# Optimization experiments

Hardware: AMD Instinct MI355X
Metric: run time of the kernel (lower is better)

## Reference

```python
import jax, jax.numpy as jnp
import numpy as np

HOP = jnp.array([0, 1, 4, 7, 2, 5, 8, 3, 6, 9, 11, 14, 10, 12, 15, 13, 16])
GRAPH = jnp.array([0, 1, 4, 7, 2, 5, 8, 3, 6, 9, 12, 10, 13, 15, 11, 14, 16])
D_MODEL, L, D_INNER, D_STATE, DT_RANK = 512, 17, 1024, 4, 32


def layernorm(x, w, b, eps=1e-5):
    mu = x.mean(-1, keepdims=True)
    var = ((x - mu) ** 2).mean(-1, keepdims=True)
    return (x - mu) * jax.lax.rsqrt(var + eps) * w + b


def setup_inputs() -> dict:
    key = jax.random.key(0)
    ks = jax.random.split(key, 9)
    B = 4096
    s = lambda k, shape: jax.random.normal(k, shape, jnp.float32) * 0.02
    # A_log init per mamba_ssm: log(1..d_state) repeated over d_inner
    A_log = jnp.log(jnp.broadcast_to(jnp.arange(1, D_STATE + 1, dtype=jnp.float32), (D_INNER, D_STATE)))
    return {
        "x": jax.random.normal(ks[0], (B, L, D_MODEL), jnp.float32),
        "bp_embed": s(ks[1], (1, 5, D_MODEL)),
        "ln_w": jnp.ones((D_MODEL,), jnp.float32),
        "ln_b": jnp.zeros((D_MODEL,), jnp.float32),
        "in_proj_w": s(ks[2], (2 * D_INNER, D_MODEL)),
        "conv_w": 1.0 + s(ks[3], (D_INNER,)),  # d_conv=1 depthwise conv == per-channel scale
        "conv_b": jnp.zeros((D_INNER,), jnp.float32),
        "x_proj_w": s(ks[4], (DT_RANK + 2 * D_STATE, D_INNER)),
        "dt_proj_w": s(ks[5], (D_INNER, DT_RANK)),
        "dt_proj_b": s(ks[6], (D_INNER,)) - 4.0,  # softplus-inverse-ish small dt init
        "A_log": A_log,
        "D": jnp.ones((D_INNER,), jnp.float32),
        "out_proj_w": s(ks[7], (D_MODEL, D_INNER)),
    }


def mamba(u, in_proj_w, conv_w, conv_b, x_proj_w, dt_proj_w, dt_proj_b, A_log, D, out_proj_w):
    # u: [B, L, d_model]
    xz = jnp.einsum('bld,ed->ble', u, in_proj_w)          # [B,L,2*d_inner]
    xm, z = jnp.split(xz, 2, axis=-1)
    xm = jax.nn.silu(xm * conv_w + conv_b)                 # d_conv=1 -> pointwise
    x_dbl = jnp.einsum('ble,fe->blf', xm, x_proj_w)        # [B,L,dt_rank+2*d_state]
    dt_r = x_dbl[..., :DT_RANK]
    Bm = x_dbl[..., DT_RANK:DT_RANK + D_STATE]
    Cm = x_dbl[..., DT_RANK + D_STATE:]
    dt = jax.nn.softplus(jnp.einsum('blr,er->ble', dt_r, dt_proj_w) + dt_proj_b)  # [B,L,d_inner]
    A = -jnp.exp(A_log)                                    # [d_inner,d_state]

    def step(h, inp):
        dt_t, B_t, C_t, x_t = inp                          # [B,di],[B,ds],[B,ds],[B,di]
        dA = jnp.exp(dt_t[..., None] * A)                  # [B,di,ds]
        h = dA * h + (dt_t * x_t)[..., None] * B_t[:, None, :]
        y = jnp.einsum('bes,bs->be', h, C_t)
        return h, y

    bsz = u.shape[0]
    h0 = jnp.zeros((bsz, D_INNER, D_STATE), u.dtype)
    seq = (dt.transpose(1, 0, 2), Bm.transpose(1, 0, 2), Cm.transpose(1, 0, 2), xm.transpose(1, 0, 2))
    _, ys = jax.lax.scan(step, h0, seq)                    # ys: [L,B,d_inner]
    y = ys.transpose(1, 0, 2) + xm * D
    y = y * jax.nn.silu(z)
    return jnp.einsum('ble,de->bld', y, out_proj_w)


def reference(x, bp_embed, ln_w, ln_b, in_proj_w, conv_w, conv_b, x_proj_w,
              dt_proj_w, dt_proj_b, A_log, D, out_proj_w):
    bp = bp_embed
    x_bpe = jnp.concatenate([bp[:, :3], bp[:, :3], bp[:, :3], bp[:, :1],
                             bp[:, 3:], bp[:, :1], bp[:, 3:], bp[:, 3:]], axis=1)  # [1,17,dim]
    x_ssm = x[:, HOP, :] + x_bpe
    x_ssm = layernorm(x_ssm, ln_w, ln_b)
    x_ssm = mamba(x_ssm, in_proj_w, conv_w, conv_b, x_proj_w,
                  dt_proj_w, dt_proj_b, A_log, D, out_proj_w)
    return x + x_ssm[:, GRAPH, :]
```

## Files before the change

kernel.cpp:

```cpp
#include <hip/hip_runtime.h>

typedef unsigned short u16;
typedef unsigned int   u32;
typedef __bf16 bf16_t;
typedef bf16_t bf16x8 __attribute__((ext_vector_type(8)));
typedef float  f32x4  __attribute__((ext_vector_type(4)));

#define DEV static __device__ __forceinline__

__constant__ int c_HOP[17] = {0,1,4,7,2,5,8,3,6,9,11,14,10,12,15,13,16};
__constant__ int c_BPE[17] = {0,1,2,0,1,2,0,1,2,0,3,4,0,3,4,3,4};

DEV u16 f2bf(float f){
  u32 x = __builtin_bit_cast(u32, f);
  x += 0x7fffu + ((x >> 16) & 1u);
  return (u16)(x >> 16);
}
DEV float bf2f(u32 u){ return __builtin_bit_cast(float, u << 16); }
DEV float silu_f(float v){ return v / (1.f + __expf(-v)); }
DEV float softplus_f(float s){ return (s > 20.f) ? s : log1pf(__expf(s)); }

DEV void gll16(const void* g, void* l){
  __builtin_amdgcn_global_load_lds((__attribute__((address_space(1))) void*)g,
                                   (__attribute__((address_space(3))) void*)l,
                                   16, 0, 0);
}

__global__ __launch_bounds__(256) void cvt4(
    const float* __restrict__ s0, u16* __restrict__ d0, int n0,
    const float* __restrict__ s1, u16* __restrict__ d1, int n1,
    const float* __restrict__ s2, u16* __restrict__ d2, int n2,
    const float* __restrict__ s3, u16* __restrict__ d3, int n3)
{
  int t = blockIdx.x * 256 + threadIdx.x;
  if (t < n0){ d0[t] = f2bf(s0[t]); return; }
  t -= n0; if (t < n1){ d1[t] = f2bf(s1[t]); return; }
  t -= n1; if (t < n2){ d2[t] = f2bf(s2[t]); return; }
  t -= n2; if (t < n3){ d3[t] = f2bf(s3[t]); }
}

__global__ __launch_bounds__(256) void ln_gather(
    const float* __restrict__ x, const float* __restrict__ bpe,
    const float* __restrict__ lnw, const float* __restrict__ lnb,
    u16* __restrict__ u)
{
  int tok = blockIdx.x;
  int b = tok / 17;
  int l = tok - b * 17;
  const float* xr = x   + ((size_t)b * 17 + c_HOP[l]) * 512;
  const float* br = bpe + (size_t)c_BPE[l] * 512;
  int tid = threadIdx.x;
  int d0 = tid * 2;
  float2 xv = *(const float2*)(xr + d0);
  float2 bv = *(const float2*)(br + d0);
  float v0 = xv.x + bv.x, v1 = xv.y + bv.y;

  __shared__ float red[8];
  float s = v0 + v1;
  #pragma unroll
  for (int o = 32; o; o >>= 1) s += __shfl_xor(s, o);
  if ((tid & 63) == 0) red[tid >> 6] = s;
  __syncthreads();
  float mu = (red[0] + red[1] + red[2] + red[3]) * (1.f / 512.f);
  float a0 = v0 - mu, a1 = v1 - mu;
  float q = a0 * a0 + a1 * a1;
  #pragma unroll
  for (int o = 32; o; o >>= 1) q += __shfl_xor(q, o);
  if ((tid & 63) == 0) red[4 + (tid >> 6)] = q;
  __syncthreads();
  float var = (red[4] + red[5] + red[6] + red[7]) * (1.f / 512.f);
  float rs = rsqrtf(var + 1e-5f);

  u16 o0 = f2bf(a0 * rs * lnw[d0]     + lnb[d0]);
  u16 o1 = f2bf(a1 * rs * lnw[d0 + 1] + lnb[d0 + 1]);
  u32 pack = (u32)o0 | ((u32)o1 << 16);
  *(u32*)(u + (size_t)tok * 512 + d0) = pack;
}

enum { EPI_SPLIT = 0, EPI_OUT = 1 };

template<int EPI>
__global__ __launch_bounds__(512, 2) void gemm256(
    const u16* __restrict__ A, int lda,
    const u16* __restrict__ W, int K, int MT,
    u16* __restrict__ ob0, u16* __restrict__ ob1,
    const float* __restrict__ p0, const float* __restrict__ p1,
    const float* __restrict__ xres, float* __restrict__ fout)
{
  __shared__ u16 smem[65536];

  int nwg = gridDim.x;
  int cpx = nwg >> 3;
  int wg = (blockIdx.x & 7) * cpx + (blockIdx.x >> 3);
  int NT = nwg / MT;
  int nt = wg % NT, mt = wg / NT;
  int brow = mt * 256, bcol = nt * 256;
  int tid = threadIdx.x, lane = tid & 63, wid = tid >> 6;
  int wm = wid >> 2, wn = wid & 3;
  int l15 = lane & 15, lhi = lane >> 4;

  f32x4 acc[8][4] = {};

  int sr0 = tid >> 2, sr1 = 128 + (tid >> 2), sch = tid & 3;
  const u16* gA0 = A + (size_t)(brow + sr0) * lda + (sch ^ ((sr0 >> 1) & 3)) * 8;
  const u16* gA1 = A + (size_t)(brow + sr1) * lda + (sch ^ ((sr1 >> 1) & 3)) * 8;
  const u16* gW0 = W + (size_t)(bcol + sr0) * K   + (sch ^ ((sr0 >> 1) & 3)) * 8;
  const u16* gW1 = W + (size_t)(bcol + sr1) * K   + (sch ^ ((sr1 >> 1) & 3)) * 8;

  auto stA = [&](int buf, int kh, int koff) {
    char* d = (char*)smem + (buf * 2 + kh) * 16384 + tid * 16;
    gll16(gA0 + koff, d);
    gll16(gA1 + koff, d + 8192);
  };
  auto stB = [&](int buf, int kh, int koff) {
    char* d = (char*)smem + 65536 + (buf * 2 + kh) * 16384 + tid * 16;
    gll16(gW0 + koff, d);
    gll16(gW1 + koff, d + 8192);
  };

  int aoff[2][4], boff[4];
  #pragma unroll
  for (int mh = 0; mh < 2; mh++)
    #pragma unroll
    for (int mi = 0; mi < 4; mi++) {
      int r = wm * 128 + mh * 64 + mi * 16 + l15;
      aoff[mh][mi] = r * 64 + ((lhi ^ ((r >> 1) & 3)) * 16);
    }
  #pragma unroll
  for (int ni = 0; ni < 4; ni++) {
    int r = wn * 64 + ni * 16 + l15;
    boff[ni] = r * 64 + ((lhi ^ ((r >> 1) & 3)) * 16);
  }

  bf16x8 bvv[4];

#define PH(BUF, KH, MH, LOADB, STMT, WAIT)                                  \
  {                                                                         \
    const char* la = (const char*)smem + ((BUF) * 2 + (KH)) * 16384;        \
    bf16x8 a0 = *(const bf16x8*)(la + aoff[MH][0]);                         \
    bf16x8 a1 = *(const bf16x8*)(la + aoff[MH][1]);                         \
    bf16x8 a2 = *(const bf16x8*)(la + aoff[MH][2]);                         \
    bf16x8 a3 = *(const bf16x8*)(la + aoff[MH][3]);                         \
    if (LOADB) {                                                            \
      const char* lb = (const char*)smem + 65536 + ((BUF) * 2 + (KH)) * 16384; \
      bvv[0] = *(const bf16x8*)(lb + boff[0]);                              \
      bvv[1] = *(const bf16x8*)(lb + boff[1]);                              \
      bvv[2] = *(const bf16x8*)(lb + boff[2]);                              \
      bvv[3] = *(const bf16x8*)(lb + boff[3]);                              \
    }                                                                       \
    STMT                                                                    \
    __builtin_amdgcn_sched_barrier(0);                                      \
    __builtin_amdgcn_s_barrier();                                           \
    __builtin_amdgcn_s_setprio(1);                                          \
    acc[(MH)*4+0][0] = __builtin_amdgcn_mfma_f32_16x16x32_bf16(a0, bvv[0], acc[(MH)*4+0][0],0,0,0); \
    acc[(MH)*4+1][0] = __builtin_amdgcn_mfma_f32_16x16x32_bf16(a1, bvv[0], acc[(MH)*4+1][0],0,0,0); \
    acc[(MH)*4+2][0] = __builtin_amdgcn_mfma_f32_16x16x32_bf16(a2, bvv[0], acc[(MH)*4+2][0],0,0,0); \
    acc[(MH)*4+3][0] = __builtin_amdgcn_mfma_f32_16x16x32_bf16(a3, bvv[0], acc[(MH)*4+3][0],0,0,0); \
    acc[(MH)*4+0][1] = __builtin_amdgcn_mfma_f32_16x16x32_bf16(a0, bvv[1], acc[(MH)*4+0][1],0,0,0); \
    acc[(MH)*4+1][1] = __builtin_amdgcn_mfma_f32_16x16x32_bf16(a1, bvv[1], acc[(MH)*4+1][1],0,0,0); \
    acc[(MH)*4+2][1] = __builtin_amdgcn_mfma_f32_16x16x32_bf16(a2, bvv[1], acc[(MH)*4+2][1],0,0,0); \
    acc[(MH)*4+3][1] = __builtin_amdgcn_mfma_f32_16x16x32_bf16(a3, bvv[1], acc[(MH)*4+3][1],0,0,0); \
    acc[(MH)*4+0][2] = __builtin_amdgcn_mfma_f32_16x16x32_bf16(a0, bvv[2], acc[(MH)*4+0][2],0,0,0); \
    acc[(MH)*4+1][2] = __builtin_amdgcn_mfma_f32_16x16x32_bf16(a1, bvv[2], acc[(MH)*4+1][2],0,0,0); \
    acc[(MH)*4+2][2] = __builtin_amdgcn_mfma_f32_16x16x32_bf16(a2, bvv[2], acc[(MH)*4+2][2],0,0,0); \
    acc[(MH)*4+3][2] = __builtin_amdgcn_mfma_f32_16x16x32_bf16(a3, bvv[2], acc[(MH)*4+3][2],0,0,0); \
    acc[(MH)*4+0][3] = __builtin_amdgcn_mfma_f32_16x16x32_bf16(a0, bvv[3], acc[(MH)*4+0][3],0,0,0); \
    acc[(MH)*4+1][3] = __builtin_amdgcn_mfma_f32_16x16x32_bf16(a1, bvv[3], acc[(MH)*4+1][3],0,0,0); \
    acc[(MH)*4+2][3] = __builtin_amdgcn_mfma_f32_16x16x32_bf16(a2, bvv[3], acc[(MH)*4+2][3],0,0,0); \
    acc[(MH)*4+3][3] = __builtin_amdgcn_mfma_f32_16x16x32_bf16(a3, bvv[3], acc[(MH)*4+3][3],0,0,0); \
    __builtin_amdgcn_s_setprio(0);                                          \
    WAIT                                                                    \
    __builtin_amdgcn_s_barrier();                                           \
    __builtin_amdgcn_sched_barrier(0);                                      \
  }

  int T = K >> 6;

  stA(0, 0, 0);  stB(0, 0, 0);
  stA(0, 1, 32); stB(0, 1, 32);
  asm volatile("s_waitcnt vmcnt(4)" ::: "memory");
  __builtin_amdgcn_s_barrier();
  __builtin_amdgcn_sched_barrier(0);

  for (int t = 0; t < T; ++t) {
    int bf = t & 1, nb = bf ^ 1;
    int nk = (t + 1) << 6;
    bool s = (t + 1 < T);
    PH(bf, 0, 0, true,  { if (s) stA(nb, 0, nk); }, {});
    if (s) {
      PH(bf, 0, 1, false, { stB(nb, 0, nk); },
         { asm volatile("s_waitcnt vmcnt(4)" ::: "memory"); });
    } else {
      PH(bf, 0, 1, false, {},
         { asm volatile("s_waitcnt vmcnt(0)" ::: "memory"); });
    }
    PH(bf, 1, 0, true,  { if (s) stA(nb, 1, nk + 32); }, {});
    if (s) {
      PH(bf, 1, 1, false, { stB(nb, 1, nk + 32); },
         { asm volatile("s_waitcnt vmcnt(4)" ::: "memory"); });
    } else {
      PH(bf, 1, 1, false, {}, {});
    }
  }
#undef PH

  if constexpr (EPI == EPI_SPLIT) {
    u16* cl = smem;
    bool isx = (bcol < 1024);
    #pragma unroll
    for (int fm = 0; fm < 8; fm++) {
      int lrow = wm * 128 + fm * 16 + lhi * 4;
      #pragma unroll
      for (int ni = 0; ni < 4; ni++) {
        int col = wn * 64 + ni * 16 + l15;
        int cidx = isx ? (bcol + col) : 0;
        float cw = isx ? p0[cidx] : 1.f;
        float cb = isx ? p1[cidx] : 0.f;
        #pragma unroll
        for (int rr = 0; rr < 4; rr++) {
          int row = lrow + rr;
          cl[row * 256 + ((col + row * 8) & 255)] =
              f2bf(silu_f(acc[fm][ni][rr] * cw + cb));
        }
      }
    }
    __syncthreads();
    int colbase = isx ? bcol : (bcol - 1024);
    u16* dst = isx ? ob0 : ob1;
    #pragma unroll
    for (int i = 0; i < 16; i++) {
      int idx = i * 512 + tid;
      int row = idx >> 5;
      int q = idx & 31;
      uint4 v = *(const uint4*)(cl + row * 256 + ((q * 8 + row * 8) & 255));
      *(uint4*)(dst + (size_t)(brow + row) * 1024 + colbase + q * 8) = v;
    }
  } else {
    float* cf = (float*)smem;
    #pragma unroll
    for (int mh = 0; mh < 2; mh++) {
      __syncthreads();
      if (wm == mh) {
        #pragma unroll
        for (int fm = 0; fm < 8; fm++) {
          int lrow = fm * 16 + lhi * 4;
          #pragma unroll
          for (int ni = 0; ni < 4; ni++) {
            int col = wn * 64 + ni * 16 + l15;
            #pragma unroll
            for (int rr = 0; rr < 4; rr++) {
              int row = lrow + rr;
              cf[row * 256 + ((col + row * 4) & 255)] = acc[fm][ni][rr];
            }
          }
        }
      }
      __syncthreads();
      #pragma unroll
      for (int i = 0; i < 16; i++) {
        int idx = i * 512 + tid;
        int row = idx >> 6;
        int q = idx & 63;
        int grow = brow + mh * 128 + row;
        u32 bq = (u32)grow / 17u;
        int gl = grow - (int)bq * 17;
        size_t orow = (size_t)bq * 17 + c_HOP[gl];
        size_t off = orow * 512 + bcol + q * 4;
        float4 xv = *(const float4*)(xres + off);
        const float* cp = cf + row * 256 + ((q * 4 + row * 4) & 255);
        float4 ov;
        ov.x = xv.x + cp[0]; ov.y = xv.y + cp[1];
        ov.z = xv.z + cp[2]; ov.w = xv.w + cp[3];
        *(float4*)(fout + off) = ov;
      }
    }
  }
}

enum { EPI_XDBL = 0, EPI_DT = 1 };

template<int EPI>
__global__ __launch_bounds__(256) void gemm_bt(
    const u16* __restrict__ A, int lda,
    const u16* __restrict__ W, int K, int MT,
    u16* __restrict__ ob0, const float* __restrict__ p0)
{
  __shared__ u16 sm[16384];
  int nwg = gridDim.x;
  int cpx = nwg >> 3;
  int wg = (blockIdx.x & 7) * cpx + (blockIdx.x >> 3);
  int NT = nwg / MT;
  int nt = wg % NT, mt = wg / NT;
  int brow = mt * 128, bcol = nt * 128;
  int tid = threadIdx.x, lane = tid & 63, wid = tid >> 6;
  int wm = wid >> 1, wn = wid & 1;

  f32x4 acc[4][4] = {};

  int srow = tid >> 2;
  int sch  = tid & 3;

  const u16* gA0 = A + (size_t)(brow + srow)      * lda + (sch ^ ((srow >> 1) & 3)) * 8;
  const u16* gA1 = A + (size_t)(brow + 64 + srow) * lda + (sch ^ (((64 + srow) >> 1) & 3)) * 8;
  const u16* gW0 = W + (size_t)(bcol + srow)      * K   + (sch ^ ((srow >> 1) & 3)) * 8;
  const u16* gW1 = W + (size_t)(bcol + 64 + srow) * K   + (sch ^ (((64 + srow) >> 1) & 3)) * 8;

  auto STAGE = [&](int buf, int kt) {
    char* dA = (char*)sm + buf * 8192 + tid * 16;
    char* dW = (char*)sm + 16384 + buf * 8192 + tid * 16;
    gll16(gA0 + kt, dA);
    gll16(gA1 + kt, dA + 4096);
    gll16(gW0 + kt, dW);
    gll16(gW1 + kt, dW + 4096);
  };

  int aoff[4], boff[4];
  #pragma unroll
  for (int mi = 0; mi < 4; mi++) {
    int r = wm * 64 + mi * 16 + (lane & 15);
    aoff[mi] = r * 64 + (((lane >> 4) ^ ((r >> 1) & 3)) * 16);
  }
  #pragma unroll
  for (int ni = 0; ni < 4; ni++) {
    int r = wn * 64 + ni * 16 + (lane & 15);
    boff[ni] = r * 64 + (((lane >> 4) ^ ((r >> 1) & 3)) * 16);
  }

  auto COMPUTE = [&](int buf) {
    const char* la = (const char*)sm + buf * 8192;
    const char* lb = (const char*)sm + 16384 + buf * 8192;
    bf16x8 av[4], bv[4];
    #pragma unroll
    for (int mi = 0; mi < 4; mi++)
      av[mi] = *(const bf16x8*)(la + aoff[mi]);
    #pragma unroll
    for (int ni = 0; ni < 4; ni++)
      bv[ni] = *(const bf16x8*)(lb + boff[ni]);
    #pragma unroll
    for (int mi = 0; mi < 4; mi++)
      #pragma unroll
      for (int ni = 0; ni < 4; ni++)
        acc[mi][ni] = __builtin_amdgcn_mfma_f32_16x16x32_bf16(
            av[mi], bv[ni], acc[mi][ni], 0, 0, 0);
  };

  int nsteps = K >> 5;
  STAGE(0, 0);
  __syncthreads();
  int cur = 0;
  for (int s = 1; s < nsteps; ++s) {
    STAGE(cur ^ 1, s << 5);
    COMPUTE(cur);
    __syncthreads();
    cur ^= 1;
  }
  COMPUTE(cur);

  int r4 = (lane >> 4) * 4;
  int cl15 = lane & 15;
  if constexpr (EPI == EPI_XDBL) {
    #pragma unroll
    for (int mi = 0; mi < 4; mi++) {
      int rowb = brow + wm * 64 + mi * 16 + r4;
      #pragma unroll
      for (int ni = 0; ni < 4; ni++) {
        int col = bcol + wn * 64 + ni * 16 + cl15;
        if (col < 40) {
          #pragma unroll
          for (int rr = 0; rr < 4; rr++)
            ob0[(size_t)(rowb + rr) * 40 + col] = f2bf(acc[mi][ni][rr]);
        }
      }
    }
  } else {
    __syncthreads();
    u16* cls = sm;
    #pragma unroll
    for (int mi = 0; mi < 4; mi++) {
      int lrow = wm * 64 + mi * 16 + r4;
      #pragma unroll
      for (int ni = 0; ni < 4; ni++) {
        int lcol = wn * 64 + ni * 16 + cl15;
        float bb = p0[bcol + lcol];
        #pragma unroll
        for (int rr = 0; rr < 4; rr++) {
          int row = lrow + rr;
          cls[row * 128 + ((lcol + row * 8) & 127)] =
              f2bf(softplus_f(acc[mi][ni][rr] + bb));
        }
      }
    }
    __syncthreads();
    #pragma unroll
    for (int i = 0; i < 8; i++) {
      int idx = i * 256 + tid;
      int row = idx >> 4;
      int q = idx & 15;
      uint4 v = *(const uint4*)(cls + row * 128 + ((q * 8 + row * 8) & 127));
      *(uint4*)(ob0 + (size_t)(brow + row) * 1024 + bcol + q * 8) = v;
    }
  }
}

__global__ __launch_bounds__(128) void scan5(
    const u16* __restrict__ xm, const u16* __restrict__ zs,
    const u16* __restrict__ xdbl, u16* __restrict__ dty,
    const float* __restrict__ A_log, const float* __restrict__ Dp)
{
  int b = blockIdx.x;
  int tid = threadIdx.x;
  int e0 = tid * 8;
  const size_t base = (size_t)b * 17 * 1024;

  float4 al = *(const float4*)(A_log + (size_t)e0 * 4);
  float A0 = -__expf(al.x), A1 = -__expf(al.y);
  float A2 = -__expf(al.z), A3 = -__expf(al.w);
  float Dv[8];
  *(float4*)(Dv)     = *(const float4*)(Dp + e0);
  *(float4*)(Dv + 4) = *(const float4*)(Dp + e0 + 4);

  const u16* xmb = xm + base + e0;
  const u16* zsb = zs + base + e0;
  u16* db = dty + base + e0;
  const u16* bcb = xdbl + (size_t)b * 680 + 32;

  float h[8][4];
  #pragma unroll
  for (int c = 0; c < 8; c++)
    #pragma unroll
    for (int s = 0; s < 4; s++) h[c][s] = 0.f;

  #pragma unroll
  for (int t = 0; t < 17; t++) {
    uint4 xr = *(const uint4*)(xmb + t * 1024);
    uint4 zr = *(const uint4*)(zsb + t * 1024);
    uint4 dr = *(const uint4*)(db + t * 1024);
    uint4 bc = *(const uint4*)(bcb + t * 40);
    float B0 = bf2f(bc.x & 0xffffu), B1 = bf2f(bc.x >> 16);
    float B2 = bf2f(bc.y & 0xffffu), B3 = bf2f(bc.y >> 16);
    float C0 = bf2f(bc.z & 0xffffu), C1 = bf2f(bc.z >> 16);
    float C2 = bf2f(bc.w & 0xffffu), C3 = bf2f(bc.w >> 16);
    u32 yo[4];
    const u32* xw = (const u32*)&xr;
    const u32* zw = (const u32*)&zr;
    const u32* dw = (const u32*)&dr;
    #pragma unroll
    for (int c = 0; c < 8; c++) {
      u32 x16 = (c & 1) ? (xw[c >> 1] >> 16) : (xw[c >> 1] & 0xffffu);
      u32 z16 = (c & 1) ? (zw[c >> 1] >> 16) : (zw[c >> 1] & 0xffffu);
      u32 d16 = (c & 1) ? (dw[c >> 1] >> 16) : (dw[c >> 1] & 0xffffu);
      float xv = bf2f(x16), zv = bf2f(z16), dtv = bf2f(d16);
      float dx = dtv * xv;
      h[c][0] = __expf(dtv * A0) * h[c][0] + dx * B0;
      h[c][1] = __expf(dtv * A1) * h[c][1] + dx * B1;
      h[c][2] = __expf(dtv * A2) * h[c][2] + dx * B2;
      h[c][3] = __expf(dtv * A3) * h[c][3] + dx * B3;
      float yv = h[c][0] * C0 + h[c][1] * C1 + h[c][2] * C2 + h[c][3] * C3;
      u16 pk = f2bf((yv + xv * Dv[c]) * zv);
      if (c & 1) yo[c >> 1] |= ((u32)pk << 16);
      else       yo[c >> 1] = (u32)pk;
    }
    *(uint4*)(db + t * 1024) = *(uint4*)yo;
  }
}

extern "C" void kernel_launch(void* const* d_in, const int* in_sizes, int n_in,
                              void* d_out, int out_size, void* d_ws, size_t ws_size,
                              hipStream_t stream) {
  const float* x     = (const float*)d_in[0];
  const float* bpe   = (const float*)d_in[1];
  const float* lnw   = (const float*)d_in[2];
  const float* lnb   = (const float*)d_in[3];
  const float* w_in  = (const float*)d_in[4];
  const float* convw = (const float*)d_in[5];
  const float* convb = (const float*)d_in[6];
  const float* w_xp  = (const float*)d_in[7];
  const float* w_dt  = (const float*)d_in[8];
  const float* b_dt  = (const float*)d_in[9];
  const float* A_log = (const float*)d_in[10];
  const float* Dp    = (const float*)d_in[11];
  const float* w_out = (const float*)d_in[12];
  float* out = (float*)d_out;

  u16* ws = (u16*)d_ws;
  u16* wb_in  = ws;
  u16* wb_out = wb_in  + 1048576;
  u16* wb_xp  = wb_out + 524288;
  u16* wb_dt  = wb_xp  + 40960;
  u16* xm     = wb_dt  + 32768;
  u16* zs     = xm     + 71303168;
  u16* xdbl   = zs     + 71303168;
  u16* dty    = xdbl   + 2785280;
  u16* u      = dty;

  const int MT2 = 272;
  const int MT1 = 544;

  cvt4<<<6432, 256, 0, stream>>>(w_in, wb_in, 1048576, w_out, wb_out, 524288,
                                 w_xp, wb_xp, 40960, w_dt, wb_dt, 32768);

  ln_gather<<<69632, 256, 0, stream>>>(x, bpe, lnw, lnb, u);

  gemm256<EPI_SPLIT><<<MT2 * 8, 512, 0, stream>>>(
      u, 512, wb_in, 512, MT2, xm, zs, convw, convb, nullptr, nullptr);

  gemm_bt<EPI_XDBL><<<MT1 * 1, 256, 0, stream>>>(
      xm, 1024, wb_xp, 1024, MT1, xdbl, nullptr);

  gemm_bt<EPI_DT><<<MT1 * 8, 256, 0, stream>>>(
      xdbl, 40, wb_dt, 32, MT1, dty, b_dt);

  scan5<<<4096, 128, 0, stream>>>(xm, zs, xdbl, dty, A_log, Dp);

  gemm256<EPI_OUT><<<MT2 * 2, 512, 0, stream>>>(
      dty, 1024, wb_out, 1024, MT2, nullptr, nullptr, nullptr, nullptr, x, out);
}
```

Baseline: 846.3 us.

## Simplify gemm256 pipeline to single-K-tile double buffer and move out_proj to 128-tile GEMM

The 256x256 GEMM loses its fine-grained four-phase interleaved pipeline and becomes a simple double-buffered loop over 32-wide K tiles. That halves LDS so four workgroups can be resident per CU, and the SPLIT epilogue is staged in two halves to fit the smaller buffer. The out_proj GEMM moves from the 256-tile kernel to the 128-tile gemm_bt kernel with a new residual-add epilogue, giving it a larger grid. MFMA blocks in gemm_bt are also wrapped in setprio. The trade is losing the carefully tuned load/compute interleaving in exchange for occupancy and better load balance on the small out_proj GEMM.

New measurement: 1.972 ms. 133% more time.

```diff
diff --git a/kernel.cpp b/kernel.cpp
--- a/kernel.cpp
+++ b/kernel.cpp
@@ -77,17 +77,16 @@
   *(u32*)(u + (size_t)tok * 512 + d0) = pack;
 }
 
-enum { EPI_SPLIT = 0, EPI_OUT = 1 };
+enum { EPI_SPLIT = 0 };
 
 template<int EPI>
-__global__ __launch_bounds__(512, 2) void gemm256(
+__global__ __launch_bounds__(512, 4) void gemm256(
     const u16* __restrict__ A, int lda,
     const u16* __restrict__ W, int K, int MT,
     u16* __restrict__ ob0, u16* __restrict__ ob1,
-    const float* __restrict__ p0, const float* __restrict__ p1,
-    const float* __restrict__ xres, float* __restrict__ fout)
+    const float* __restrict__ p0, const float* __restrict__ p1)
 {
-  __shared__ u16 smem[65536];
+  __shared__ u16 smem[32768];
 
   int nwg = gridDim.x;
   int cpx = nwg >> 3;
@@ -107,15 +106,13 @@
   const u16* gW0 = W + (size_t)(bcol + sr0) * K   + (sch ^ ((sr0 >> 1) & 3)) * 8;
   const u16* gW1 = W + (size_t)(bcol + sr1) * K   + (sch ^ ((sr1 >> 1) & 3)) * 8;
 
-  auto stA = [&](int buf, int kh, int koff) {
-    char* d = (char*)smem + (buf * 2 + kh) * 16384 + tid * 16;
-    gll16(gA0 + koff, d);
-    gll16(gA1 + koff, d + 8192);
-  };
-  auto stB = [&](int buf, int kh, int koff) {
-    char* d = (char*)smem + 65536 + (buf * 2 + kh) * 16384 + tid * 16;
-    gll16(gW0 + koff, d);
-    gll16(gW1 + koff, d + 8192);
+  auto STAGE = [&](int buf, int koff) {
+    char* dA = (char*)smem + buf * 16384 + tid * 16;
+    char* dB = (char*)smem + 32768 + buf * 16384 + tid * 16;
+    gll16(gA0 + koff, dA);
+    gll16(gA1 + koff, dA + 8192);
+    gll16(gW0 + koff, dB);
+    gll16(gW1 + koff, dB + 8192);
   };
 
   int aoff[2][4], boff[4];
@@ -132,114 +129,56 @@
     boff[ni] = r * 64 + ((lhi ^ ((r >> 1) & 3)) * 16);
   }
 
-  bf16x8 bvv[4];
-
-#define PH(BUF, KH, MH, LOADB, STMT, WAIT)                                  \
-  {                                                                         \
-    const char* la = (const char*)smem + ((BUF) * 2 + (KH)) * 16384;        \
-    bf16x8 a0 = *(const bf16x8*)(la + aoff[MH][0]);                         \
-    bf16x8 a1 = *(const bf16x8*)(la + aoff[MH][1]);                         \
-    bf16x8 a2 = *(const bf16x8*)(la + aoff[MH][2]);                         \
-    bf16x8 a3 = *(const bf16x8*)(la + aoff[MH][3]);                         \
-    if (LOADB) {                                                            \
-      const char* lb = (const char*)smem + 65536 + ((BUF) * 2 + (KH)) * 16384; \
-      bvv[0] = *(const bf16x8*)(lb + boff[0]);                              \
-      bvv[1] = *(const bf16x8*)(lb + boff[1]);                              \
-      bvv[2] = *(const bf16x8*)(lb + boff[2]);                              \
-      bvv[3] = *(const bf16x8*)(lb + boff[3]);                              \
-    }                                                                       \
-    STMT                                                                    \
-    __builtin_amdgcn_sched_barrier(0);                                      \
-    __builtin_amdgcn_s_barrier();                                           \
-    __builtin_amdgcn_s_setprio(1);                                          \
-    acc[(MH)*4+0][0] = __builtin_amdgcn_mfma_f32_16x16x32_bf16(a0, bvv[0], acc[(MH)*4+0][0],0,0,0); \
-    acc[(MH)*4+1][0] = __builtin_amdgcn_mfma_f32_16x16x32_bf16(a1, bvv[0], acc[(MH)*4+1][0],0,0,0); \
-    acc[(MH)*4+2][0] = __builtin_amdgcn_mfma_f32_16x16x32_bf16(a2, bvv[0], acc[(MH)*4+2][0],0,0,0); \
-    acc[(MH)*4+3][0] = __builtin_amdgcn_mfma_f32_16x16x32_bf16(a3, bvv[0], acc[(MH)*4+3][0],0,0,0); \
-    acc[(MH)*4+0][1] = __builtin_amdgcn_mfma_f32_16x16x32_bf16(a0, bvv[1], acc[(MH)*4+0][1],0,0,0); \
-    acc[(MH)*4+1][1] = __builtin_amdgcn_mfma_f32_16x16x32_bf16(a1, bvv[1], acc[(MH)*4+1][1],0,0,0); \
-    acc[(MH)*4+2][1] = __builtin_amdgcn_mfma_f32_16x16x32_bf16(a2, bvv[1], acc[(MH)*4+2][1],0,0,0); \
-    acc[(MH)*4+3][1] = __builtin_amdgcn_mfma_f32_16x16x32_bf16(a3, bvv[1], acc[(MH)*4+3][1],0,0,0); \
-    acc[(MH)*4+0][2] = __builtin_amdgcn_mfma_f32_16x16x32_bf16(a0, bvv[2], acc[(MH)*4+0][2],0,0,0); \
-    acc[(MH)*4+1][2] = __builtin_amdgcn_mfma_f32_16x16x32_bf16(a1, bvv[2], acc[(MH)*4+1][2],0,0,0); \
-    acc[(MH)*4+2][2] = __builtin_amdgcn_mfma_f32_16x16x32_bf16(a2, bvv[2], acc[(MH)*4+2][2],0,0,0); \
-    acc[(MH)*4+3][2] = __builtin_amdgcn_mfma_f32_16x16x32_bf16(a3, bvv[2], acc[(MH)*4+3][2],0,0,0); \
-    acc[(MH)*4+0][3] = __builtin_amdgcn_mfma_f32_16x16x32_bf16(a0, bvv[3], acc[(MH)*4+0][3],0,0,0); \
-    acc[(MH)*4+1][3] = __builtin_amdgcn_mfma_f32_16x16x32_bf16(a1, bvv[3], acc[(MH)*4+1][3],0,0,0); \
-    acc[(MH)*4+2][3] = __builtin_amdgcn_mfma_f32_16x16x32_bf16(a2, bvv[3], acc[(MH)*4+2][3],0,0,0); \
-    acc[(MH)*4+3][3] = __builtin_amdgcn_mfma_f32_16x16x32_bf16(a3, bvv[3], acc[(MH)*4+3][3],0,0,0); \
-    __builtin_amdgcn_s_setprio(0);                                          \
-    WAIT                                                                    \
-    __builtin_amdgcn_s_barrier();                                           \
-    __builtin_amdgcn_sched_barrier(0);                                      \
-  }
-
-  int T = K >> 6;
-
-  stA(0, 0, 0);  stB(0, 0, 0);
-  stA(0, 1, 32); stB(0, 1, 32);
-  asm volatile("s_waitcnt vmcnt(4)" ::: "memory");
-  __builtin_amdgcn_s_barrier();
-  __builtin_amdgcn_sched_barrier(0);
-
+  auto COMPUTE = [&](int buf) {
+    const char* la = (const char*)smem + buf * 16384;
+    const char* lb = (const char*)smem + 32768 + buf * 16384;
+    bf16x8 bv0 = *(const bf16x8*)(lb + boff[0]);
+    bf16x8 bv1 = *(const bf16x8*)(lb + boff[1]);
+    bf16x8 bv2 = *(const bf16x8*)(lb + boff[2]);
+    bf16x8 bv3 = *(const bf16x8*)(lb + boff[3]);
+    __builtin_amdgcn_s_setprio(1);
+    #pragma unroll
+    for (int mh = 0; mh < 2; mh++) {
+      bf16x8 a0 = *(const bf16x8*)(la + aoff[mh][0]);
+      bf16x8 a1 = *(const bf16x8*)(la + aoff[mh][1]);
+      bf16x8 a2 = *(const bf16x8*)(la + aoff[mh][2]);
+      bf16x8 a3 = *(const bf16x8*)(la + aoff[mh][3]);
+      acc[mh*4+0][0] = __builtin_amdgcn_mfma_f32_16x16x32_bf16(a0, bv0, acc[mh*4+0][0],0,0,0);
+      acc[mh*4+1][0] = __builtin_amdgcn_mfma_f32_16x16x32_bf16(a1, bv0, acc[mh*4+1][0],0,0,0);
+      acc[mh*4+2][0] = __builtin_amdgcn_mfma_f32_16x16x32_bf16(a2, bv0, acc[mh*4+2][0],0,0,0);
+      acc[mh*4+3][0] = __builtin_amdgcn_mfma_f32_16x16x32_bf16(a3, bv0, acc[mh*4+3][0],0,0,0);
+      acc[mh*4+0][1] = __builtin_amdgcn_mfma_f32_16x16x32_bf16(a0, bv1, acc[mh*4+0][1],0,0,0);
+      acc[mh*4+1][1] = __builtin_amdgcn_mfma_f32_16x16x32_bf16(a1, bv1, acc[mh*4+1][1],0,0,0);
+      acc[mh*4+2][1] = __builtin_amdgcn_mfma_f32_16x16x32_bf16(a2, bv1, acc[mh*4+2][1],0,0,0);
+      acc[mh*4+3][1] = __builtin_amdgcn_mfma_f32_16x16x32_bf16(a3, bv1, acc[mh*4+3][1],0,0,0);
+      acc[mh*4+0][2] = __builtin_amdgcn_mfma_f32_16x16x32_bf16(a0, bv2, acc[mh*4+0][2],0,0,0);
+      acc[mh*4+1][2] = __builtin_amdgcn_mfma_f32_16x16x32_bf16(a1, bv2, acc[mh*4+1][2],0,0,0);
+      acc[mh*4+2][2] = __builtin_amdgcn_mfma_f32_16x16x32_bf16(a2, bv2, acc[mh*4+2][2],0,0,0);
+      acc[mh*4+3][2] = __builtin_amdgcn_mfma_f32_16x16x32_bf16(a3, bv2, acc[mh*4+3][2],0,0,0);
+      acc[mh*4+0][3] = __builtin_amdgcn_mfma_f32_16x16x32_bf16(a0, bv3, acc[mh*4+0][3],0,0,0);
+      acc[mh*4+1][3] = __builtin_amdgcn_mfma_f32_16x16x32_bf16(a1, bv3, acc[mh*4+1][3],0,0,0);
+      acc[mh*4+2][3] = __builtin_amdgcn_mfma_f32_16x16x32_bf16(a2, bv3, acc[mh*4+2][3],0,0,0);
+      acc[mh*4+3][3] = __builtin_amdgcn_mfma_f32_16x16x32_bf16(a3, bv3, acc[mh*4+3][3],0,0,0);
+    }
+    __builtin_amdgcn_s_setprio(0);
+  };
+
+  int T = K >> 5;
+  STAGE(0, 0);
+  __syncthreads();
   for (int t = 0; t < T; ++t) {
-    int bf = t & 1, nb = bf ^ 1;
-    int nk = (t + 1) << 6;
-    bool s = (t + 1 < T);
-    PH(bf, 0, 0, true,  { if (s) stA(nb, 0, nk); }, {});
-    if (s) {
-      PH(bf, 0, 1, false, { stB(nb, 0, nk); },
-         { asm volatile("s_waitcnt vmcnt(4)" ::: "memory"); });
-    } else {
-      PH(bf, 0, 1, false, {},
-         { asm volatile("s_waitcnt vmcnt(0)" ::: "memory"); });
-    }
-    PH(bf, 1, 0, true,  { if (s) stA(nb, 1, nk + 32); }, {});
-    if (s) {
-      PH(bf, 1, 1, false, { stB(nb, 1, nk + 32); },
-         { asm volatile("s_waitcnt vmcnt(4)" ::: "memory"); });
-    } else {
-      PH(bf, 1, 1, false, {}, {});
-    }
-  }
-#undef PH
-
-  if constexpr (EPI == EPI_SPLIT) {
+    if (t + 1 < T) STAGE((t + 1) & 1, (t + 1) << 5);
+    COMPUTE(t & 1);
+    __syncthreads();
+  }
+
+  {
     u16* cl = smem;
     bool isx = (bcol < 1024);
-    #pragma unroll
-    for (int fm = 0; fm < 8; fm++) {
-      int lrow = wm * 128 + fm * 16 + lhi * 4;
-      #pragma unroll
-      for (int ni = 0; ni < 4; ni++) {
-        int col = wn * 64 + ni * 16 + l15;
-        int cidx = isx ? (bcol + col) : 0;
-        float cw = isx ? p0[cidx] : 1.f;
-        float cb = isx ? p1[cidx] : 0.f;
-        #pragma unroll
-        for (int rr = 0; rr < 4; rr++) {
-          int row = lrow + rr;
-          cl[row * 256 + ((col + row * 8) & 255)] =
-              f2bf(silu_f(acc[fm][ni][rr] * cw + cb));
-        }
-      }
-    }
-    __syncthreads();
     int colbase = isx ? bcol : (bcol - 1024);
     u16* dst = isx ? ob0 : ob1;
     #pragma unroll
-    for (int i = 0; i < 16; i++) {
-      int idx = i * 512 + tid;
-      int row = idx >> 5;
-      int q = idx & 31;
-      uint4 v = *(const uint4*)(cl + row * 256 + ((q * 8 + row * 8) & 255));
-      *(uint4*)(dst + (size_t)(brow + row) * 1024 + colbase + q * 8) = v;
-    }
-  } else {
-    float* cf = (float*)smem;
-    #pragma unroll
     for (int mh = 0; mh < 2; mh++) {
-      __syncthreads();
       if (wm == mh) {
         #pragma unroll
         for (int fm = 0; fm < 8; fm++) {
@@ -247,43 +186,40 @@
           #pragma unroll
           for (int ni = 0; ni < 4; ni++) {
             int col = wn * 64 + ni * 16 + l15;
+            int cidx = isx ? (bcol + col) : 0;
+            float cw = isx ? p0[cidx] : 1.f;
+            float cb = isx ? p1[cidx] : 0.f;
             #pragma unroll
             for (int rr = 0; rr < 4; rr++) {
               int row = lrow + rr;
-              cf[row * 256 + ((col + row * 4) & 255)] = acc[fm][ni][rr];
+              cl[row * 256 + ((col + row * 8) & 255)] =
+                  f2bf(silu_f(acc[fm][ni][rr] * cw + cb));
             }
           }
         }
       }
       __syncthreads();
       #pragma unroll
-      for (int i = 0; i < 16; i++) {
+      for (int i = 0; i < 8; i++) {
         int idx = i * 512 + tid;
-        int row = idx >> 6;
-        int q = idx & 63;
-        int grow = brow + mh * 128 + row;
-        u32 bq = (u32)grow / 17u;
-        int gl = grow - (int)bq * 17;
-        size_t orow = (size_t)bq * 17 + c_HOP[gl];
-        size_t off = orow * 512 + bcol + q * 4;
-        float4 xv = *(const float4*)(xres + off);
-        const float* cp = cf + row * 256 + ((q * 4 + row * 4) & 255);
-        float4 ov;
-        ov.x = xv.x + cp[0]; ov.y = xv.y + cp[1];
-        ov.z = xv.z + cp[2]; ov.w = xv.w + cp[3];
-        *(float4*)(fout + off) = ov;
-      }
-    }
-  }
-}
-
-enum { EPI_XDBL = 0, EPI_DT = 1 };
+        int row = idx >> 5;
+        int q = idx & 31;
+        uint4 v = *(const uint4*)(cl + row * 256 + ((q * 8 + row * 8) & 255));
+        *(uint4*)(dst + (size_t)(brow + mh * 128 + row) * 1024 + colbase + q * 8) = v;
+      }
+      __syncthreads();
+    }
+  }
+}
+
+enum { EPI_XDBL = 0, EPI_DT = 1, EPI_OUT = 2 };
 
 template<int EPI>
 __global__ __launch_bounds__(256) void gemm_bt(
     const u16* __restrict__ A, int lda,
     const u16* __restrict__ W, int K, int MT,
-    u16* __restrict__ ob0, const float* __restrict__ p0)
+    u16* __restrict__ ob0, const float* __restrict__ p0,
+    const float* __restrict__ xres, float* __restrict__ fout)
 {
   __shared__ u16 sm[16384];
   int nwg = gridDim.x;
@@ -336,12 +272,14 @@
     #pragma unroll
     for (int ni = 0; ni < 4; ni++)
       bv[ni] = *(const bf16x8*)(lb + boff[ni]);
+    __builtin_amdgcn_s_setprio(1);
     #pragma unroll
     for (int mi = 0; mi < 4; mi++)
       #pragma unroll
       for (int ni = 0; ni < 4; ni++)
         acc[mi][ni] = __builtin_amdgcn_mfma_f32_16x16x32_bf16(
             av[mi], bv[ni], acc[mi][ni], 0, 0, 0);
+    __builtin_amdgcn_s_setprio(0);
   };
 
   int nsteps = K >> 5;
@@ -372,7 +310,7 @@
         }
       }
     }
-  } else {
+  } else if constexpr (EPI == EPI_DT) {
     __syncthreads();
     u16* cls = sm;
     #pragma unroll
@@ -398,6 +336,46 @@
       int q = idx & 15;
       uint4 v = *(const uint4*)(cls + row * 128 + ((q * 8 + row * 8) & 127));
       *(uint4*)(ob0 + (size_t)(brow + row) * 1024 + bcol + q * 8) = v;
+    }
+  } else {
+    __syncthreads();
+    float* cf = (float*)sm;
+    #pragma unroll
+    for (int mh = 0; mh < 2; mh++) {
+      if (wm == mh) {
+        #pragma unroll
+        for (int mi = 0; mi < 4; mi++) {
+          int lrow = mi * 16 + r4;
+          #pragma unroll
+          for (int ni = 0; ni < 4; ni++) {
+            int col = wn * 64 + ni * 16 + cl15;
+            #pragma unroll
+            for (int rr = 0; rr < 4; rr++) {
+              int row = lrow + rr;
+              cf[row * 128 + ((col + row * 4) & 127)] = acc[mi][ni][rr];
+            }
+          }
+        }
+      }
+      __syncthreads();
+      #pragma unroll
+      for (int i = 0; i < 8; i++) {
+        int idx = i * 256 + tid;
+        int row = idx >> 5;
+        int q = idx & 31;
+        int grow = brow + mh * 64 + row;
+        u32 bq = (u32)grow / 17u;
+        int gl = grow - (int)bq * 17;
+        size_t orow = (size_t)bq * 17 + c_HOP[gl];
+        size_t off = orow * 512 + bcol + q * 4;
+        float4 xv = *(const float4*)(xres + off);
+        const float* cp = cf + row * 128 + ((q * 4 + row * 4) & 127);
+        float4 ov;
+        ov.x = xv.x + cp[0]; ov.y = xv.y + cp[1];
+        ov.z = xv.z + cp[2]; ov.w = xv.w + cp[3];
+        *(float4*)(fout + off) = ov;
+      }
+      __syncthreads();
     }
   }
 }
@@ -502,16 +480,16 @@
   ln_gather<<<69632, 256, 0, stream>>>(x, bpe, lnw, lnb, u);
 
   gemm256<EPI_SPLIT><<<MT2 * 8, 512, 0, stream>>>(
-      u, 512, wb_in, 512, MT2, xm, zs, convw, convb, nullptr, nullptr);
+      u, 512, wb_in, 512, MT2, xm, zs, convw, convb);
 
   gemm_bt<EPI_XDBL><<<MT1 * 1, 256, 0, stream>>>(
-      xm, 1024, wb_xp, 1024, MT1, xdbl, nullptr);
+      xm, 1024, wb_xp, 1024, MT1, xdbl, nullptr, nullptr, nullptr);
 
   gemm_bt<EPI_DT><<<MT1 * 8, 256, 0, stream>>>(
-      xdbl, 40, wb_dt, 32, MT1, dty, b_dt);
+      xdbl, 40, wb_dt, 32, MT1, dty, b_dt, nullptr, nullptr);
 
   scan5<<<4096, 128, 0, stream>>>(xm, zs, xdbl, dty, A_log, Dp);
 
-  gemm256<EPI_OUT><<<MT2 * 2, 512, 0, stream>>>(
-      dty, 1024, wb_out, 1024, MT2, nullptr, nullptr, nullptr, nullptr, x, out);
-}
+  gemm_bt<EPI_OUT><<<MT1 * 4, 256, 0, stream>>>(
+      dty, 1024, wb_out, 1024, MT1, nullptr, nullptr, x, out);
+}
```
